# Kernel tuning notes

Hardware: AMD Instinct MI355X
Metric: run time of the kernel (lower is better)

Reference implementation:

```python
import jax, jax.numpy as jnp
import numpy as np

N = 1024
DH = 64   # XH feature dim (<= DOUT)
DP = 32   # XP feature dim
DIN = 64  # input_dim (== output_dim, required by f_psi applied to vij)
DOUT = 64 # output_dim
BN_EPS = 1e-5
SIGMA = 0.1


def setup_inputs() -> dict:
    key = jax.random.key(0)
    ks = jax.random.split(key, 8)
    return {
        "XH": jax.random.normal(ks[0], (N, DH), dtype=jnp.float32),
        "XP": jax.random.normal(ks[1], (N, DP), dtype=jnp.float32),
        "XX": jax.random.normal(ks[2], (N, DIN), dtype=jnp.float32),
        "K": 16,
        # nn.Parameter weight/bias: normal(0, 0.01)
        "weight": 0.01 * jax.random.normal(ks[3], (DIN, DOUT), dtype=jnp.float32),
        "bias": 0.01 * jax.random.normal(ks[4], (DOUT,), dtype=jnp.float32),
        # f_psi Linear params (torch kaiming-uniform ~ small uniform)
        "psi_w": jax.random.uniform(ks[5], (DOUT, DIN), dtype=jnp.float32, minval=-1.0, maxval=1.0) / np.sqrt(DIN),
        "psi_b": jax.random.uniform(ks[6], (DOUT,), dtype=jnp.float32, minval=-1.0, maxval=1.0) / np.sqrt(DIN),
        # BatchNorm1d affine params
        "gamma": jnp.ones((DOUT,), dtype=jnp.float32),
        "beta": jnp.zeros((DOUT,), dtype=jnp.float32),
    }


def _pairwise_norm(X):
    # [N, N] matrix of L2 norms of row differences (as in torch.norm(X[:,None]-X, dim=2))
    return jnp.linalg.norm(X[:, None, :] - X[None, :, :], axis=2)


def _adjacency(XH, XP, K, sigma=SIGMA):
    eps = float(np.finfo(np.float64).eps)
    XHs = XH / (sigma + eps)
    WHo = _pairwise_norm(XHs)
    WH = jnp.exp(-((WHo - WHo.min()) / (WHo.max() - WHo.min())) / 2)
    Wlo = _pairwise_norm(XP)
    Wl = jnp.exp(-((Wlo - Wlo.min()) / (Wlo.max() - Wlo.min())))
    WW = WH + 0.2 * Wl
    _, idx = jax.lax.top_k(WW, K)                       # per-row top-K neighbors
    n = WW.shape[0]
    mask = jnp.zeros_like(WW).at[jnp.arange(n)[:, None], idx].set(1.0)
    mask = mask + mask.T                                # symmetrize
    # Original sets Adj=WW/WW=1 where mask!=0 and Adj=WW-WW=0 elsewhere -> binary adjacency
    return (mask > 0).astype(WW.dtype)


def reference(XH, XP, XX, K, weight, bias, psi_w, psi_b, gamma, beta):
    Adj = _adjacency(XH, XP, K)                         # [N, N], {0,1}
    x = XX @ weight                                     # [N, D]
    vi = x[None, :, :] * Adj[:, :, None]                # [N, N, D]: vi[i,j] = x[j]*Adj[i,j]
    vij = x[None, :, :] + vi                            # [N, N, D]
    # f_psi: Linear -> BatchNorm1d (training-mode batch stats) -> Sigmoid, over N*N rows
    h = jnp.einsum('ijd,ed->ije', vij, psi_w) + psi_b   # [N, N, D]
    mu = h.mean(axis=(0, 1))                            # [D]
    var = h.var(axis=(0, 1))                            # biased var, as torch BN
    att = jax.nn.sigmoid((h - mu) * jax.lax.rsqrt(var + BN_EPS) * gamma + beta)
    # self-loop attention forced to 1 on the diagonal
    eye = jnp.eye(x.shape[0], dtype=bool)[:, :, None]
    att = jnp.where(eye, jnp.float32(1.0), att)
    out = (att * vi).sum(axis=0) + bias                 # [N, D]
    return (out[:, :XH.shape[1]], XP, out)
```

## Files before the change

kernel.cpp:

```cpp
#include <hip/hip_runtime.h>
#include <hip/hip_fp16.h>
#include <cfloat>

#define NN 1024


__global__ __launch_bounds__(256) void gcn_transpose(const float* __restrict__ XH,
                                                     const float* __restrict__ XP,
                                                     float* __restrict__ XHT,
                                                     float* __restrict__ XPT) {
    const int j0 = blockIdx.x * 64;
    const int tid = threadIdx.x;
    __shared__ float th[64][65];
    __shared__ float tp[32][65];
#pragma unroll
    for (int it = 0; it < 16; ++it) {
        int idx = it * 256 + tid;
        int jl = idx >> 6, d = idx & 63;
        th[d][jl] = XH[(j0 + jl) * 64 + d];
    }
#pragma unroll
    for (int it = 0; it < 8; ++it) {
        int idx = it * 256 + tid;
        int jl = idx >> 5, d = idx & 31;
        tp[d][jl] = XP[(j0 + jl) * 32 + d];
    }
    __syncthreads();
#pragma unroll
    for (int it = 0; it < 16; ++it) {
        int idx = it * 256 + tid;
        int d = idx >> 6, jl = idx & 63;
        XHT[d * NN + j0 + jl] = th[d][jl];
    }
#pragma unroll
    for (int it = 0; it < 8; ++it) {
        int idx = it * 256 + tid;
        int d = idx >> 6, jl = idx & 63;
        XPT[d * NN + j0 + jl] = tp[d][jl];
    }
}

__global__ __launch_bounds__(256) void gcn_dist(const float* __restrict__ XH,
                                                const float* __restrict__ XP,
                                                const float* __restrict__ XHT,
                                                const float* __restrict__ XPT,
                                                __half2* __restrict__ dist,
                                                unsigned* __restrict__ maxbits) {
    const int b = blockIdx.x;
    const int i0 = (b >> 2) * 4;
    const int j = (b & 3) * 256 + threadIdx.x;
    const int tid = threadIdx.x;
    __shared__ float shi[4][64];
    __shared__ float spi[4][32];
    shi[tid >> 6][tid & 63] = XH[(i0 + (tid >> 6)) * 64 + (tid & 63)];
    if (tid < 128) spi[tid >> 5][tid & 31] = XP[(i0 + (tid >> 5)) * 32 + (tid & 31)];
    __syncthreads();
    float dh[4] = {0.f, 0.f, 0.f, 0.f}, dp[4] = {0.f, 0.f, 0.f, 0.f};
#pragma unroll 16
    for (int d = 0; d < 64; ++d) {
        float v = XHT[d * NN + j];
#pragma unroll
        for (int r = 0; r < 4; ++r) { float t = v - shi[r][d]; dh[r] += t * t; }
    }
#pragma unroll 16
    for (int d = 0; d < 32; ++d) {
        float v = XPT[d * NN + j];
#pragma unroll
        for (int r = 0; r < 4; ++r) { float t = v - spi[r][d]; dp[r] += t * t; }
    }
#pragma unroll
    for (int r = 0; r < 4; ++r)
        dist[(size_t)(i0 + r) * NN + j] =
            __halves2half2(__float2half(sqrtf(dh[r])), __float2half(sqrtf(dp[r])));
    float mh = fmaxf(fmaxf(dh[0], dh[1]), fmaxf(dh[2], dh[3]));
    float mp = fmaxf(fmaxf(dp[0], dp[1]), fmaxf(dp[2], dp[3]));
#pragma unroll
    for (int m = 1; m < 64; m <<= 1) {
        mh = fmaxf(mh, __shfl_xor(mh, m));
        mp = fmaxf(mp, __shfl_xor(mp, m));
    }
    __shared__ float wmx[4][2];
    if ((tid & 63) == 0) { wmx[tid >> 6][0] = mh; wmx[tid >> 6][1] = mp; }
    __syncthreads();
    if (tid == 0) {
        float a = fmaxf(fmaxf(wmx[0][0], wmx[1][0]), fmaxf(wmx[2][0], wmx[3][0]));
        float b2 = fmaxf(fmaxf(wmx[0][1], wmx[1][1]), fmaxf(wmx[2][1], wmx[3][1]));
        atomicMax(&maxbits[0], __float_as_uint(a));
        atomicMax(&maxbits[32], __float_as_uint(b2));
    }
}

__global__ __launch_bounds__(256) void gcn_topk(const __half2* __restrict__ dist,
                                                const unsigned* __restrict__ maxbits,
                                                const int* __restrict__ kptr,
                                                int* __restrict__ eidx,
                                                int* __restrict__ indeg) {
    const int tid = threadIdx.x;
    const int w = tid >> 6, lane = tid & 63;
    const int i = blockIdx.x * 4 + w;
    const float cH = -0.5f / sqrtf(__uint_as_float(maxbits[0]));
    const float cP = -1.0f / sqrtf(__uint_as_float(maxbits[32]));
    const float4* drow = (const float4*)(dist + (size_t)i * NN);
    unsigned kk[16];
#pragma unroll
    for (int s = 0; s < 4; ++s) {
        float4 v = drow[s * 64 + lane];
        const __half2* hp = (const __half2*)&v;
#pragma unroll
        for (int q = 0; q < 4; ++q) {
            float nh = __low2float(hp[q]);
            float np = __high2float(hp[q]);
            float wwv = __expf(nh * cH) + 0.2f * __expf(np * cP);
            int j = s * 256 + lane * 4 + q;
            kk[s * 4 + q] = (__float_as_uint(wwv) & 0xFFFFFC00u) | (unsigned)(1023 - j);
        }
    }
    const int K = *kptr;
    int jsave = 0;
    for (int t = 0; t < K; ++t) {
        unsigned bk = 0;
#pragma unroll
        for (int v = 0; v < 16; ++v) bk = kk[v] > bk ? kk[v] : bk;
#pragma unroll
        for (int m = 1; m < 64; m <<= 1) {
            unsigned o = (unsigned)__shfl_xor((int)bk, m);
            bk = o > bk ? o : bk;
        }
        int j = 1023 - (int)(bk & 0x3FFu);
        if (lane == t) jsave = j;
        if (((j >> 2) & 63) == lane) {
            int slot = ((j >> 8) << 2) | (j & 3);
#pragma unroll
            for (int v = 0; v < 16; ++v)
                if (v == slot) kk[v] = 0u;
        }
    }
    if (lane < K) {
        eidx[i * 16 + lane] = jsave;
        atomicAdd(&indeg[jsave], 1);
    }
}

__global__ __launch_bounds__(256) void gcn_overlap(const int* __restrict__ eidx,
                                                   int* __restrict__ overlap) {
    const int gid = blockIdx.x * 256 + threadIdx.x;
    const int i = gid >> 4;
    const int j = eidx[gid];
    if (j < 0) return;
    const int4* ej = (const int4*)(eidx + j * 16);
    bool rec = false;
#pragma unroll
    for (int q = 0; q < 4; ++q) {
        int4 e = ej[q];
        rec |= (e.x == i) | (e.y == i) | (e.z == i) | (e.w == i);
    }
    if (rec) atomicAdd(&overlap[j], 1);
}

__global__ __launch_bounds__(256) void gcn_degree(const int* __restrict__ indeg,
                                                  const int* __restrict__ overlap,
                                                  const int* __restrict__ kptr,
                                                  int* __restrict__ cdeg) {
    const int j = blockIdx.x * 256 + threadIdx.x;
    if (j < NN) cdeg[j] = *kptr + indeg[j] - overlap[j];
}

__global__ __launch_bounds__(64) void gcn_xy(const float* __restrict__ XX,
                                             const float* __restrict__ W,
                                             const float* __restrict__ psi_w,
                                             float* __restrict__ x,
                                             float* __restrict__ y) {
    const int i = blockIdx.x;
    const int e = threadIdx.x;
    __shared__ float xin[64], xs[64];
    xin[e] = XX[i * 64 + e];
    __syncthreads();
    float acc = 0.f;
#pragma unroll
    for (int d = 0; d < 64; ++d) acc += xin[d] * W[d * 64 + e];
    xs[e] = acc;
    x[i * 64 + e] = acc;
    __syncthreads();
    float acc2 = 0.f;
    const float* pw = psi_w + e * 64;
#pragma unroll
    for (int d = 0; d < 64; ++d) acc2 += xs[d] * pw[d];
    y[i * 64 + e] = acc2;
}

__global__ __launch_bounds__(256) void gcn_stats(const float* __restrict__ y,
                                                 const int* __restrict__ cdeg,
                                                 const float* __restrict__ gamma,
                                                 float* __restrict__ m0out,
                                                 float* __restrict__ scaleout) {
    const int e = blockIdx.x;
    const int tid = threadIdx.x;
    __shared__ double r1[256], r2[256];
    double s1 = 0.0, s2 = 0.0;
    for (int j = tid; j < NN; j += 256) {
        double t = (double)y[j * 64 + e];
        int c = cdeg[j];
        s1 += (double)(NN + c) * t;
        s2 += (double)(NN + 3 * c) * t * t;
    }
    r1[tid] = s1; r2[tid] = s2;
    __syncthreads();
    for (int k = 128; k > 0; k >>= 1) {
        if (tid < k) { r1[tid] += r1[tid + k]; r2[tid] += r2[tid + k]; }
        __syncthreads();
    }
    if (tid == 0) {
        double m = r1[0] / 1048576.0;
        double var = r2[0] / 1048576.0 - m * m;
        m0out[e] = (float)m;
        scaleout[e] = (float)(1.0 / sqrt(var + 1e-5)) * gamma[e];
    }
}

__global__ __launch_bounds__(64) void gcn_out(const float* __restrict__ x,
                                              const float* __restrict__ y,
                                              const int* __restrict__ cdeg,
                                              const float* __restrict__ beta,
                                              const float* __restrict__ m0,
                                              const float* __restrict__ scale,
                                              const float* __restrict__ bias,
                                              const float* __restrict__ XP,
                                              float* __restrict__ out) {
    const int j = blockIdx.x;
    const int e = threadIdx.x;
    float t = y[j * 64 + e];
    float z = (2.f * t - m0[e]) * scale[e] + beta[e];
    float s = 1.f / (1.f + expf(-z));
    float val = x[j * 64 + e] * ((float)(cdeg[j] - 1) * s + 1.f) + bias[e];
    out[j * 64 + e] = val;
    out[98304 + j * 64 + e] = val;
    if (e < 32) out[65536 + j * 32 + e] = XP[j * 32 + e];
}

extern "C" void kernel_launch(void* const* d_in, const int* in_sizes, int n_in,
                              void* d_out, int out_size, void* d_ws, size_t ws_size,
                              hipStream_t stream) {
    const float* XH    = (const float*)d_in[0];
    const float* XP    = (const float*)d_in[1];
    const float* XX    = (const float*)d_in[2];
    const int*   Kp    = (const int*)d_in[3];
    const float* W     = (const float*)d_in[4];
    const float* bias  = (const float*)d_in[5];
    const float* psi_w = (const float*)d_in[6];
    const float* psi_b = (const float*)d_in[7];
    const float* gamma = (const float*)d_in[8];
    const float* beta  = (const float*)d_in[9];
    (void)psi_b;
    float* out = (float*)d_out;
    char* ws = (char*)d_ws;

    __half2* dist     = (__half2*)ws;
    float* XHT        = (float*)(ws + 0x400000);
    float* XPT        = (float*)(ws + 0x440000);
    int* eidx         = (int*)(ws + 0x460000);
    int* indeg        = (int*)(ws + 0x470000);
    int* overlap      = (int*)(ws + 0x471000);
    unsigned* maxbits = (unsigned*)(ws + 0x472000);
    int* cdeg         = (int*)(ws + 0x473000);
    float* m0         = (float*)(ws + 0x474000);
    float* scale      = (float*)(ws + 0x474200);
    float* x          = (float*)(ws + 0x480000);
    float* y          = (float*)(ws + 0x4C0000);

    hipMemsetAsync(ws + 0x460000, 0xFF, 0x10000, stream);
    hipMemsetAsync(ws + 0x470000, 0x00, 0x3000, stream);

    gcn_transpose<<<dim3(16), dim3(256), 0, stream>>>(XH, XP, XHT, XPT);
    gcn_dist<<<dim3(1024), dim3(256), 0, stream>>>(XH, XP, XHT, XPT, dist, maxbits);
    gcn_topk<<<dim3(256), dim3(256), 0, stream>>>(dist, maxbits, Kp, eidx, indeg);
    gcn_overlap<<<dim3(64), dim3(256), 0, stream>>>(eidx, overlap);
    gcn_degree<<<dim3(4), dim3(256), 0, stream>>>(indeg, overlap, Kp, cdeg);
    gcn_xy<<<dim3(1024), dim3(64), 0, stream>>>(XX, W, psi_w, x, y);
    gcn_stats<<<dim3(64), dim3(256), 0, stream>>>(y, cdeg, gamma, m0, scale);
    gcn_out<<<dim3(1024), dim3(64), 0, stream>>>(x, y, cdeg, beta, m0, scale, bias, XP, out);
}
```

Measured before the change: 142.7 us.

## Fold memsets, degree and stats kernels into neighbours; store fp32 distances

Removes the two memsets. Workspace zeroing moves into the transpose kernel and the degree init into the dist kernel, so the gcn_degree pass disappears: cdeg is built directly through atomics in topk and overlap. The separate BN stats kernel is replaced by double-precision atomic accumulation into 32 bins inside gcn_xy, followed by a tiny one-block finalize. Distances are now stored as two fp32 arrays instead of packed half2, and the top-k keys become 64-bit so the full weight is kept without bit truncation. This doubles the distance buffer traffic and adds atomic contention, in exchange for fewer launches.

```diff
diff --git a/kernel.cpp b/kernel.cpp
--- a/kernel.cpp
+++ b/kernel.cpp
@@ -1,5 +1,4 @@
 #include <hip/hip_runtime.h>
-#include <hip/hip_fp16.h>
 #include <cfloat>
 
 #define NN 1024
@@ -8,9 +7,14 @@
 __global__ __launch_bounds__(256) void gcn_transpose(const float* __restrict__ XH,
                                                      const float* __restrict__ XP,
                                                      float* __restrict__ XHT,
-                                                     float* __restrict__ XPT) {
-    const int j0 = blockIdx.x * 64;
+                                                     float* __restrict__ XPT,
+                                                     unsigned* __restrict__ maxbits,
+                                                     double* __restrict__ Sbins) {
+    const int b = blockIdx.x;
+    const int j0 = b * 64;
     const int tid = threadIdx.x;
+    Sbins[b * 256 + tid] = 0.0;
+    if (b == 0 && tid < 64) maxbits[tid] = 0u;
     __shared__ float th[64][65];
     __shared__ float tp[32][65];
 #pragma unroll
@@ -44,12 +48,16 @@
                                                 const float* __restrict__ XP,
                                                 const float* __restrict__ XHT,
                                                 const float* __restrict__ XPT,
-                                                __half2* __restrict__ dist,
-                                                unsigned* __restrict__ maxbits) {
+                                                float* __restrict__ dhp,
+                                                float* __restrict__ dpp,
+                                                unsigned* __restrict__ maxbits,
+                                                const int* __restrict__ kptr,
+                                                int* __restrict__ cdeg) {
     const int b = blockIdx.x;
     const int i0 = (b >> 2) * 4;
     const int j = (b & 3) * 256 + threadIdx.x;
     const int tid = threadIdx.x;
+    if (b < 4) cdeg[j] = *kptr;
     __shared__ float shi[4][64];
     __shared__ float spi[4][32];
     shi[tid >> 6][tid & 63] = XH[(i0 + (tid >> 6)) * 64 + (tid & 63)];
@@ -69,9 +77,10 @@
         for (int r = 0; r < 4; ++r) { float t = v - spi[r][d]; dp[r] += t * t; }
     }
 #pragma unroll
-    for (int r = 0; r < 4; ++r)
-        dist[(size_t)(i0 + r) * NN + j] =
-            __halves2half2(__float2half(sqrtf(dh[r])), __float2half(sqrtf(dp[r])));
+    for (int r = 0; r < 4; ++r) {
+        dhp[(size_t)(i0 + r) * NN + j] = sqrtf(dh[r]);
+        dpp[(size_t)(i0 + r) * NN + j] = sqrtf(dp[r]);
+    }
     float mh = fmaxf(fmaxf(dh[0], dh[1]), fmaxf(dh[2], dh[3]));
     float mp = fmaxf(fmaxf(dp[0], dp[1]), fmaxf(dp[2], dp[3]));
 #pragma unroll
@@ -90,59 +99,62 @@
     }
 }
 
-__global__ __launch_bounds__(256) void gcn_topk(const __half2* __restrict__ dist,
+__global__ __launch_bounds__(256) void gcn_topk(const float* __restrict__ dhp,
+                                                const float* __restrict__ dpp,
                                                 const unsigned* __restrict__ maxbits,
                                                 const int* __restrict__ kptr,
                                                 int* __restrict__ eidx,
-                                                int* __restrict__ indeg) {
+                                                int* __restrict__ cdeg) {
     const int tid = threadIdx.x;
     const int w = tid >> 6, lane = tid & 63;
     const int i = blockIdx.x * 4 + w;
     const float cH = -0.5f / sqrtf(__uint_as_float(maxbits[0]));
     const float cP = -1.0f / sqrtf(__uint_as_float(maxbits[32]));
-    const float4* drow = (const float4*)(dist + (size_t)i * NN);
-    unsigned kk[16];
+    const float4* dh4 = (const float4*)(dhp + (size_t)i * NN);
+    const float4* dp4 = (const float4*)(dpp + (size_t)i * NN);
+    unsigned long long kk[16];
 #pragma unroll
     for (int s = 0; s < 4; ++s) {
-        float4 v = drow[s * 64 + lane];
-        const __half2* hp = (const __half2*)&v;
-#pragma unroll
-        for (int q = 0; q < 4; ++q) {
-            float nh = __low2float(hp[q]);
-            float np = __high2float(hp[q]);
-            float wwv = __expf(nh * cH) + 0.2f * __expf(np * cP);
-            int j = s * 256 + lane * 4 + q;
-            kk[s * 4 + q] = (__float_as_uint(wwv) & 0xFFFFFC00u) | (unsigned)(1023 - j);
-        }
+        float4 a = dh4[s * 64 + lane];
+        float4 b = dp4[s * 64 + lane];
+        float w0 = __expf(a.x * cH) + 0.2f * __expf(b.x * cP);
+        float w1 = __expf(a.y * cH) + 0.2f * __expf(b.y * cP);
+        float w2 = __expf(a.z * cH) + 0.2f * __expf(b.z * cP);
+        float w3 = __expf(a.w * cH) + 0.2f * __expf(b.w * cP);
+        int jb = s * 256 + lane * 4;
+        kk[s * 4 + 0] = ((unsigned long long)__float_as_uint(w0) << 32) | (unsigned)(1023 - (jb + 0));
+        kk[s * 4 + 1] = ((unsigned long long)__float_as_uint(w1) << 32) | (unsigned)(1023 - (jb + 1));
+        kk[s * 4 + 2] = ((unsigned long long)__float_as_uint(w2) << 32) | (unsigned)(1023 - (jb + 2));
+        kk[s * 4 + 3] = ((unsigned long long)__float_as_uint(w3) << 32) | (unsigned)(1023 - (jb + 3));
     }
     const int K = *kptr;
     int jsave = 0;
     for (int t = 0; t < K; ++t) {
-        unsigned bk = 0;
+        unsigned long long bk = 0ull;
 #pragma unroll
         for (int v = 0; v < 16; ++v) bk = kk[v] > bk ? kk[v] : bk;
 #pragma unroll
         for (int m = 1; m < 64; m <<= 1) {
-            unsigned o = (unsigned)__shfl_xor((int)bk, m);
+            unsigned long long o = __shfl_xor(bk, m);
             bk = o > bk ? o : bk;
         }
-        int j = 1023 - (int)(bk & 0x3FFu);
+        int j = 1023 - (int)(bk & 0x3FFull);
         if (lane == t) jsave = j;
         if (((j >> 2) & 63) == lane) {
             int slot = ((j >> 8) << 2) | (j & 3);
 #pragma unroll
             for (int v = 0; v < 16; ++v)
-                if (v == slot) kk[v] = 0u;
+                if (v == slot) kk[v] = 0ull;
         }
     }
     if (lane < K) {
         eidx[i * 16 + lane] = jsave;
-        atomicAdd(&indeg[jsave], 1);
+        atomicAdd(&cdeg[jsave], 1);
     }
 }
 
 __global__ __launch_bounds__(256) void gcn_overlap(const int* __restrict__ eidx,
-                                                   int* __restrict__ overlap) {
+                                                   int* __restrict__ cdeg) {
     const int gid = blockIdx.x * 256 + threadIdx.x;
     const int i = gid >> 4;
     const int j = eidx[gid];
@@ -154,22 +166,17 @@
         int4 e = ej[q];
         rec |= (e.x == i) | (e.y == i) | (e.z == i) | (e.w == i);
     }
-    if (rec) atomicAdd(&overlap[j], 1);
-}
-
-__global__ __launch_bounds__(256) void gcn_degree(const int* __restrict__ indeg,
-                                                  const int* __restrict__ overlap,
-                                                  const int* __restrict__ kptr,
-                                                  int* __restrict__ cdeg) {
-    const int j = blockIdx.x * 256 + threadIdx.x;
-    if (j < NN) cdeg[j] = *kptr + indeg[j] - overlap[j];
+    if (rec) atomicSub(&cdeg[j], 1);
 }
 
 __global__ __launch_bounds__(64) void gcn_xy(const float* __restrict__ XX,
                                              const float* __restrict__ W,
                                              const float* __restrict__ psi_w,
+                                             const int* __restrict__ cdeg,
                                              float* __restrict__ x,
-                                             float* __restrict__ y) {
+                                             float* __restrict__ y,
+                                             double* __restrict__ S1,
+                                             double* __restrict__ S2) {
     const int i = blockIdx.x;
     const int e = threadIdx.x;
     __shared__ float xin[64], xs[64];
@@ -186,35 +193,26 @@
 #pragma unroll
     for (int d = 0; d < 64; ++d) acc2 += xs[d] * pw[d];
     y[i * 64 + e] = acc2;
-}
-
-__global__ __launch_bounds__(256) void gcn_stats(const float* __restrict__ y,
-                                                 const int* __restrict__ cdeg,
-                                                 const float* __restrict__ gamma,
-                                                 float* __restrict__ m0out,
-                                                 float* __restrict__ scaleout) {
-    const int e = blockIdx.x;
-    const int tid = threadIdx.x;
-    __shared__ double r1[256], r2[256];
+    const int c = cdeg[i];
+    const int bin = (i & 31) * 64 + e;
+    double yd = (double)acc2;
+    atomicAdd(&S1[bin], (double)(NN + c) * yd);
+    atomicAdd(&S2[bin], (double)(NN + 3 * c) * yd * yd);
+}
+
+__global__ __launch_bounds__(64) void gcn_statsfin(const double* __restrict__ S1,
+                                                   const double* __restrict__ S2,
+                                                   const float* __restrict__ gamma,
+                                                   float* __restrict__ m0,
+                                                   float* __restrict__ scale) {
+    const int e = threadIdx.x;
     double s1 = 0.0, s2 = 0.0;
-    for (int j = tid; j < NN; j += 256) {
-        double t = (double)y[j * 64 + e];
-        int c = cdeg[j];
-        s1 += (double)(NN + c) * t;
-        s2 += (double)(NN + 3 * c) * t * t;
-    }
-    r1[tid] = s1; r2[tid] = s2;
-    __syncthreads();
-    for (int k = 128; k > 0; k >>= 1) {
-        if (tid < k) { r1[tid] += r1[tid + k]; r2[tid] += r2[tid + k]; }
-        __syncthreads();
-    }
-    if (tid == 0) {
-        double m = r1[0] / 1048576.0;
-        double var = r2[0] / 1048576.0 - m * m;
-        m0out[e] = (float)m;
-        scaleout[e] = (float)(1.0 / sqrt(var + 1e-5)) * gamma[e];
-    }
+#pragma unroll
+    for (int b = 0; b < 32; ++b) { s1 += S1[b * 64 + e]; s2 += S2[b * 64 + e]; }
+    double m = s1 / 1048576.0;
+    double var = s2 / 1048576.0 - m * m;
+    m0[e] = (float)m;
+    scale[e] = (float)(1.0 / sqrt(var + 1e-5)) * gamma[e];
 }
 
 __global__ __launch_bounds__(64) void gcn_out(const float* __restrict__ x,
@@ -254,28 +252,25 @@
     float* out = (float*)d_out;
     char* ws = (char*)d_ws;
 
-    __half2* dist     = (__half2*)ws;
-    float* XHT        = (float*)(ws + 0x400000);
-    float* XPT        = (float*)(ws + 0x440000);
-    int* eidx         = (int*)(ws + 0x460000);
-    int* indeg        = (int*)(ws + 0x470000);
-    int* overlap      = (int*)(ws + 0x471000);
-    unsigned* maxbits = (unsigned*)(ws + 0x472000);
-    int* cdeg         = (int*)(ws + 0x473000);
-    float* m0         = (float*)(ws + 0x474000);
-    float* scale      = (float*)(ws + 0x474200);
-    float* x          = (float*)(ws + 0x480000);
-    float* y          = (float*)(ws + 0x4C0000);
-
-    hipMemsetAsync(ws + 0x460000, 0xFF, 0x10000, stream);
-    hipMemsetAsync(ws + 0x470000, 0x00, 0x3000, stream);
-
-    gcn_transpose<<<dim3(16), dim3(256), 0, stream>>>(XH, XP, XHT, XPT);
-    gcn_dist<<<dim3(1024), dim3(256), 0, stream>>>(XH, XP, XHT, XPT, dist, maxbits);
-    gcn_topk<<<dim3(256), dim3(256), 0, stream>>>(dist, maxbits, Kp, eidx, indeg);
-    gcn_overlap<<<dim3(64), dim3(256), 0, stream>>>(eidx, overlap);
-    gcn_degree<<<dim3(4), dim3(256), 0, stream>>>(indeg, overlap, Kp, cdeg);
-    gcn_xy<<<dim3(1024), dim3(64), 0, stream>>>(XX, W, psi_w, x, y);
-    gcn_stats<<<dim3(64), dim3(256), 0, stream>>>(y, cdeg, gamma, m0, scale);
+    float* dhp        = (float*)ws;
+    float* dpp        = (float*)(ws + 0x400000);
+    float* XHT        = (float*)(ws + 0x800000);
+    float* XPT        = (float*)(ws + 0x840000);
+    int* eidx         = (int*)(ws + 0x860000);
+    unsigned* maxbits = (unsigned*)(ws + 0x870000);
+    int* cdeg         = (int*)(ws + 0x871000);
+    double* S1        = (double*)(ws + 0x872000);
+    double* S2        = (double*)(ws + 0x876000);
+    float* m0         = (float*)(ws + 0x87A000);
+    float* scale      = (float*)(ws + 0x87A200);
+    float* x          = (float*)(ws + 0x880000);
+    float* y          = (float*)(ws + 0x8C0000);
+
+    gcn_transpose<<<dim3(16), dim3(256), 0, stream>>>(XH, XP, XHT, XPT, maxbits, S1);
+    gcn_dist<<<dim3(1024), dim3(256), 0, stream>>>(XH, XP, XHT, XPT, dhp, dpp, maxbits, Kp, cdeg);
+    gcn_topk<<<dim3(256), dim3(256), 0, stream>>>(dhp, dpp, maxbits, Kp, eidx, cdeg);
+    gcn_overlap<<<dim3(64), dim3(256), 0, stream>>>(eidx, cdeg);
+    gcn_xy<<<dim3(1024), dim3(64), 0, stream>>>(XX, W, psi_w, cdeg, x, y, S1, S2);
+    gcn_statsfin<<<dim3(1), dim3(64), 0, stream>>>(S1, S2, gamma, m0, scale);
     gcn_out<<<dim3(1024), dim3(64), 0, stream>>>(x, y, cdeg, beta, m0, scale, bias, XP, out);
 }
```

Result: no change. 144.3 us (median of 2 runs) (+1.1%).
